# Optimization experiments

Measured on AMD Instinct MI355X. Metric: run time of the kernel, lower is better.

Reference implementation:

```python
import jax, jax.numpy as jnp
import numpy as np

SCALING = 128.0 / 64  # alpha / rank = 2.0
EPS = 1e-8


def setup_inputs() -> dict:
    key = jax.random.key(0)
    ks = jax.random.split(key, 5)
    B, S, D_IN, D_OUT, R = 2, 4096, 4096, 4096, 64
    x = jax.random.normal(ks[0], (B, S, D_IN), dtype=jnp.float32)
    base_output = jax.random.normal(ks[1], (B, S, D_OUT), dtype=jnp.float32)
    base_weight = jax.random.normal(ks[2], (D_OUT, D_IN), dtype=jnp.float32) * 0.02
    lora_A = jax.random.normal(ks[3], (R, D_IN), dtype=jnp.float32) * 0.02
    lora_B = jax.random.normal(ks[4], (D_OUT, R), dtype=jnp.float32) * 0.02
    magnitude = jnp.ones((D_OUT,), dtype=jnp.float32)
    return {"x": x, "base_output": base_output, "base_weight": base_weight,
            "lora_A": lora_A, "lora_B": lora_B, "magnitude": magnitude}


def reference(x, base_output, base_weight, lora_A, lora_B, magnitude):
    # LoRA path: x @ A^T @ B^T, scaled  (dropout p=0 -> identity)
    xa = jnp.einsum('bsd,rd->bsr', x, lora_A)          # [B,S,r]
    delta_v = jnp.einsum('bsr,or->bso', xa, lora_B) * SCALING  # [B,S,out]
    # Updated weight and its per-row L2 norm
    updated_weight = base_weight + (lora_B @ lora_A) * SCALING  # [out,in]
    updated_norm = jnp.sqrt(jnp.sum(updated_weight * updated_weight, axis=1))  # [out]
    mag_scale = magnitude / (updated_norm + EPS)  # [out]
    combined = base_output + delta_v
    return combined * mag_scale[None, None, :]
```

## Files before the change

### kernel.cpp

```cpp
#include <hip/hip_runtime.h>
#include <math.h>

typedef __bf16 bf16x8 __attribute__((ext_vector_type(8)));
typedef float f32x4 __attribute__((ext_vector_type(4)));

#define MFMA16(a, b, c) __builtin_amdgcn_mfma_f32_16x16x32_bf16(a, b, c, 0, 0, 0)

static constexpr int M_TOT = 8192;
static constexpr int DIN = 4096;
static constexpr int DOUT = 4096;
static constexpr int RNK = 64;

__device__ inline unsigned short f2bf(float f) {
    union { float f; unsigned u; } v; v.f = f;
    unsigned r = v.u + 0x7FFFu + ((v.u >> 16) & 1u);
    return (unsigned short)(r >> 16);
}

__global__ __launch_bounds__(256) void k_prep(const float* __restrict__ A,
                                              const float* __restrict__ B,
                                              unsigned short* __restrict__ Afrag,
                                              unsigned short* __restrict__ Atfrag,
                                              unsigned short* __restrict__ Bfrag) {
    int i = blockIdx.x * 256 + threadIdx.x;
    unsigned short ab = f2bf(A[i]);
    int n = i >> 12, k = i & 4095;
    Afrag[(((k >> 5) << 2) + (n >> 4)) * 512 +
          ((((k >> 3) & 3) << 4) + (n & 15)) * 8 + (k & 7)] = ab;
    Atfrag[(((k >> 4) << 1) + (n >> 5)) * 512 +
           ((((n >> 3) & 3) << 4) + (k & 15)) * 8 + (n & 7)] = ab;
    unsigned short bb = f2bf(B[i]);
    int o = i >> 6, r = i & 63;
    Bfrag[(((o >> 4) << 1) + (r >> 5)) * 512 +
          ((((r >> 3) & 3) << 4) + (o & 15)) * 8 + (r & 7)] = bb;
}

__global__ __launch_bounds__(256, 4) void k1_xa(const float* __restrict__ x,
                                                const unsigned short* __restrict__ Afrag,
                                                float* __restrict__ pxa) {
    __shared__ __align__(16) char smem[33024];
    unsigned short (*stage)[1032] = (unsigned short (*)[1032])smem;
    float (*red)[1024] = (float (*)[1024])smem;
    int tid = threadIdx.x;
    int wid = tid >> 6, lane = tid & 63;
    int row = lane & 15, kq = lane >> 4;
    int lane8 = lane * 8;
    int mt = blockIdx.x & 511, kpart = blockIdx.x >> 9;
    int m0 = mt * 16;
    int sr = tid >> 4, sc = (tid & 15) * 4;

    const float* xp = x + (size_t)(m0 + sr) * DIN + kpart * 1024 + sc;
    f32x4 r[16];
    #pragma unroll
    for (int p = 0; p < 16; ++p) r[p] = *(const f32x4*)(xp + p * 64);

    #pragma unroll
    for (int p = 0; p < 16; ++p) {
        ushort4 h;
        h.x = f2bf(r[p][0]); h.y = f2bf(r[p][1]); h.z = f2bf(r[p][2]); h.w = f2bf(r[p][3]);
        *(ushort4*)&stage[sr][p * 64 + sc] = h;
    }
    __syncthreads();

    f32x4 acc0 = {0.f, 0.f, 0.f, 0.f};
    f32x4 acc1 = acc0, acc2 = acc0, acc3 = acc0;
    #pragma unroll
    for (int s = 0; s < 8; ++s) {
        bf16x8 af = *(const bf16x8*)&stage[row][wid * 256 + s * 32 + kq * 8];
        int ks = kpart * 32 + wid * 8 + s;
        const unsigned short* ap = Afrag + (size_t)(ks << 2) * 512 + lane8;
        acc0 = MFMA16(af, *(const bf16x8*)(ap), acc0);
        acc1 = MFMA16(af, *(const bf16x8*)(ap + 512), acc1);
        acc2 = MFMA16(af, *(const bf16x8*)(ap + 1024), acc2);
        acc3 = MFMA16(af, *(const bf16x8*)(ap + 1536), acc3);
    }
    __syncthreads();

    int mb = kq * 4;
    #pragma unroll
    for (int rg = 0; rg < 4; ++rg) {
        red[wid][(mb + rg) * 64 + row]      = acc0[rg];
        red[wid][(mb + rg) * 64 + 16 + row] = acc1[rg];
        red[wid][(mb + rg) * 64 + 32 + row] = acc2[rg];
        red[wid][(mb + rg) * 64 + 48 + row] = acc3[rg];
    }
    __syncthreads();
    #pragma unroll
    for (int e = tid; e < 1024; e += 256) {
        float s = red[0][e] + red[1][e] + red[2][e] + red[3][e];
        pxa[(size_t)kpart * M_TOT * RNK + (size_t)(m0 + (e >> 6)) * RNK + (e & 63)] = s;
    }
}

__global__ __launch_bounds__(256) void k1_fin(const float* __restrict__ pxa,
                                              unsigned short* __restrict__ xafrag) {
    int tid = threadIdx.x;
    int mt = blockIdx.x;
    int e0 = tid * 4;
    size_t o = (size_t)(mt * 16 + (e0 >> 6)) * RNK + (e0 & 63);
    f32x4 s0 = *(const f32x4*)(pxa + o);
    f32x4 s1 = *(const f32x4*)(pxa + (size_t)M_TOT * RNK + o);
    f32x4 s2 = *(const f32x4*)(pxa + 2 * (size_t)M_TOT * RNK + o);
    f32x4 s3 = *(const f32x4*)(pxa + 3 * (size_t)M_TOT * RNK + o);
    int ml = e0 >> 6, r0 = e0 & 63;
    ushort4 h;
    h.x = f2bf(s0[0] + s1[0] + s2[0] + s3[0]);
    h.y = f2bf(s0[1] + s1[1] + s2[1] + s3[1]);
    h.z = f2bf(s0[2] + s1[2] + s2[2] + s3[2]);
    h.w = f2bf(s0[3] + s1[3] + s2[3] + s3[3]);
    *(ushort4*)&xafrag[((size_t)(mt * 2 + (r0 >> 5))) * 512 +
                       ((((r0 >> 3) & 3) << 4) + ml) * 8 + (r0 & 7)] = h;
}

__global__ __launch_bounds__(256, 4) void k2_norm(const float* __restrict__ bw,
                                                  const unsigned short* __restrict__ Bfrag,
                                                  const unsigned short* __restrict__ Atfrag,
                                                  float* __restrict__ pn) {
    __shared__ __align__(16) char smem[33280];
    float (*stagef)[516] = (float (*)[516])smem;
    float (*part)[16] = (float (*)[16])(smem + 33024);
    int tid = threadIdx.x;
    int wid = tid >> 6, lane = tid & 63;
    int row = lane & 15, kq = lane >> 4;
    int lane8 = lane * 8;
    int ot = blockIdx.x & 255, ipart = blockIdx.x >> 8;
    int o0 = ot * 16;
    int sr = tid >> 4, sc = (tid & 15) * 4;

    const float* bwp = bw + (size_t)(o0 + sr) * DIN + ipart * 512 + sc;
    f32x4 q[8];
    #pragma unroll
    for (int p = 0; p < 8; ++p) q[p] = *(const f32x4*)(bwp + p * 64);

    bf16x8 b0 = *(const bf16x8*)(Bfrag + (size_t)(ot * 2) * 512 + lane8);
    bf16x8 b1 = *(const bf16x8*)(Bfrag + (size_t)(ot * 2 + 1) * 512 + lane8);

    #pragma unroll
    for (int p = 0; p < 8; ++p) *(f32x4*)&stagef[sr][p * 64 + sc] = q[p];
    __syncthreads();

    f32x4 nacc = {0.f, 0.f, 0.f, 0.f};
    #pragma unroll
    for (int g = 0; g < 8; ++g) {
        int iloc = wid * 128 + g * 16;
        int it = (ipart * 512 + iloc) >> 4;
        const unsigned short* atp = Atfrag + (size_t)(it * 2) * 512 + lane8;
        bf16x8 a0 = *(const bf16x8*)(atp);
        bf16x8 a1 = *(const bf16x8*)(atp + 512);
        f32x4 d = {0.f, 0.f, 0.f, 0.f};
        d = MFMA16(a0, b0, d);
        d = MFMA16(a1, b1, d);
        f32x4 wv = *(const f32x4*)&stagef[row][iloc + kq * 4];
        #pragma unroll
        for (int rg = 0; rg < 4; ++rg) {
            float w = wv[rg] + 2.0f * d[rg];
            nacc[rg] += w * w;
        }
    }
    float ns = nacc[0] + nacc[1] + nacc[2] + nacc[3];
    ns += __shfl_xor(ns, 16, 64);
    ns += __shfl_xor(ns, 32, 64);
    if (kq == 0) part[wid][row] = ns;
    __syncthreads();
    if (tid < 16)
        pn[ipart * DOUT + o0 + tid] =
            part[0][tid] + part[1][tid] + part[2][tid] + part[3][tid];
}

__global__ __launch_bounds__(256) void k2b_scale(const float* __restrict__ pn,
                                                 const float* __restrict__ mag,
                                                 float* __restrict__ mscale) {
    int o = blockIdx.x * 256 + threadIdx.x;
    float n2 = 0.f;
    #pragma unroll
    for (int p = 0; p < 8; ++p) n2 += pn[p * DOUT + o];
    mscale[o] = mag[o] / (sqrtf(n2) + 1e-8f);
}

__global__ __launch_bounds__(256) void kB(const float* __restrict__ base,
                                          const unsigned short* __restrict__ xafrag,
                                          const unsigned short* __restrict__ Bfrag,
                                          const float* __restrict__ mscale,
                                          float* __restrict__ out) {
    __shared__ float dls[32][260];
    int tid = threadIdx.x;
    int wid = tid >> 6, lane = tid & 63;
    int row = lane & 15, kq = lane >> 4;
    int m0 = blockIdx.x * 32;
    int n0 = blockIdx.y * 256;
    int col = n0 + lane * 4;
    int lane8 = lane * 8;

    f32x4 bpre[2][4];
    #pragma unroll
    for (int h = 0; h < 2; ++h)
        #pragma unroll
        for (int r = 0; r < 4; ++r)
            bpre[h][r] = __builtin_nontemporal_load(
                (const f32x4*)(base + (size_t)(m0 + h * 16 + wid * 4 + r) * DOUT + col));
    f32x4 msv = *(const f32x4*)(mscale + col);

    bf16x8 xb0[2], xb1[2];
    #pragma unroll
    for (int h = 0; h < 2; ++h) {
        size_t mt = (size_t)(blockIdx.x * 2 + h);
        xb0[h] = *(const bf16x8*)(xafrag + (mt * 2) * 512 + lane8);
        xb1[h] = *(const bf16x8*)(xafrag + (mt * 2 + 1) * 512 + lane8);
    }

    #pragma unroll
    for (int nt = 0; nt < 4; ++nt) {
        size_t ntg = (size_t)((n0 + wid * 64 + nt * 16) >> 4);
        bf16x8 a0 = *(const bf16x8*)(Bfrag + (ntg * 2) * 512 + lane8);
        bf16x8 a1 = *(const bf16x8*)(Bfrag + (ntg * 2 + 1) * 512 + lane8);
        #pragma unroll
        for (int h = 0; h < 2; ++h) {
            f32x4 acc = {0.f, 0.f, 0.f, 0.f};
            acc = MFMA16(a0, xb0[h], acc);
            acc = MFMA16(a1, xb1[h], acc);
            *(f32x4*)&dls[h * 16 + row][wid * 64 + nt * 16 + kq * 4] = acc;
        }
    }
    __syncthreads();

    #pragma unroll
    for (int h = 0; h < 2; ++h)
        #pragma unroll
        for (int r = 0; r < 4; ++r) {
            int m = h * 16 + wid * 4 + r;
            f32x4 d = *(const f32x4*)&dls[m][lane * 4];
            size_t gidx = (size_t)(m0 + m) * DOUT + col;
            f32x4 o;
            #pragma unroll
            for (int j = 0; j < 4; ++j) o[j] = (bpre[h][r][j] + 2.0f * d[j]) * msv[j];
            __builtin_nontemporal_store(o, (f32x4*)(out + gidx));
        }
}

extern "C" void kernel_launch(void* const* d_in, const int* in_sizes, int n_in,
                              void* d_out, int out_size, void* d_ws, size_t ws_size,
                              hipStream_t stream) {
    const float* x    = (const float*)d_in[0];
    const float* base = (const float*)d_in[1];
    const float* bw   = (const float*)d_in[2];
    const float* lA   = (const float*)d_in[3];
    const float* lB   = (const float*)d_in[4];
    const float* mag  = (const float*)d_in[5];
    float* out = (float*)d_out;

    char* ws = (char*)d_ws;
    unsigned short* Afrag  = (unsigned short*)(ws);
    unsigned short* Atfrag = (unsigned short*)(ws + (512u << 10));
    unsigned short* Bfrag  = (unsigned short*)(ws + (1024u << 10));
    unsigned short* xafrag = (unsigned short*)(ws + (1536u << 10));
    float*          pxa    = (float*)(ws + (2560u << 10));
    float*          pn     = (float*)(ws + (10752u << 10));
    float*          msc    = (float*)(ws + (10880u << 10));

    hipLaunchKernelGGL(k_prep, dim3(1024), dim3(256), 0, stream, lA, lB, Afrag, Atfrag, Bfrag);
    hipLaunchKernelGGL(k1_xa, dim3(2048), dim3(256), 0, stream, x, Afrag, pxa);
    hipLaunchKernelGGL(k2_norm, dim3(2048), dim3(256), 0, stream, bw, Bfrag, Atfrag, pn);
    hipLaunchKernelGGL(k1_fin, dim3(512), dim3(256), 0, stream, pxa, xafrag);
    hipLaunchKernelGGL(k2b_scale, dim3(DOUT / 256), dim3(256), 0, stream, pn, mag, msc);
    hipLaunchKernelGGL(kB, dim3(M_TOT / 32, DOUT / 256), dim3(256), 0, stream,
                       base, xafrag, Bfrag, msc, out);
}
```

Measured before the change: 124.0 us.

## Halve split-K in xa and norm kernels with register-prefetched chunk loop

k1_xa and k2_norm now cover twice the K range per block in four chunks, loading the next chunk into registers while the current chunk's MFMAs run. The split-K factor drops from 4 to 2 for xa and from 8 to 4 for the norm, so fewer partial sums are written and re-read by the finalize kernels. Shared memory per block is halved. The cost is half as many blocks (1024 each), an extra barrier per chunk, and the occupancy hint removed from launch_bounds.

```diff
diff --git a/kernel.cpp b/kernel.cpp
--- a/kernel.cpp
+++ b/kernel.cpp
@@ -35,11 +35,11 @@
           ((((r >> 3) & 3) << 4) + (o & 15)) * 8 + (r & 7)] = bb;
 }
 
-__global__ __launch_bounds__(256, 4) void k1_xa(const float* __restrict__ x,
-                                                const unsigned short* __restrict__ Afrag,
-                                                float* __restrict__ pxa) {
-    __shared__ __align__(16) char smem[33024];
-    unsigned short (*stage)[1032] = (unsigned short (*)[1032])smem;
+__global__ __launch_bounds__(256) void k1_xa(const float* __restrict__ x,
+                                             const unsigned short* __restrict__ Afrag,
+                                             float* __restrict__ pxa) {
+    __shared__ __align__(16) char smem[16640];
+    unsigned short (*stage)[520] = (unsigned short (*)[520])smem;
     float (*red)[1024] = (float (*)[1024])smem;
     int tid = threadIdx.x;
     int wid = tid >> 6, lane = tid & 63;
@@ -49,30 +49,40 @@
     int m0 = mt * 16;
     int sr = tid >> 4, sc = (tid & 15) * 4;
 
-    const float* xp = x + (size_t)(m0 + sr) * DIN + kpart * 1024 + sc;
-    f32x4 r[16];
-    #pragma unroll
-    for (int p = 0; p < 16; ++p) r[p] = *(const f32x4*)(xp + p * 64);
-
-    #pragma unroll
-    for (int p = 0; p < 16; ++p) {
-        ushort4 h;
-        h.x = f2bf(r[p][0]); h.y = f2bf(r[p][1]); h.z = f2bf(r[p][2]); h.w = f2bf(r[p][3]);
-        *(ushort4*)&stage[sr][p * 64 + sc] = h;
-    }
-    __syncthreads();
+    const float* xp = x + (size_t)(m0 + sr) * DIN + kpart * 2048 + sc;
+
+    f32x4 r[8];
+    #pragma unroll
+    for (int p = 0; p < 8; ++p) r[p] = *(const f32x4*)(xp + p * 64);
 
     f32x4 acc0 = {0.f, 0.f, 0.f, 0.f};
     f32x4 acc1 = acc0, acc2 = acc0, acc3 = acc0;
-    #pragma unroll
-    for (int s = 0; s < 8; ++s) {
-        bf16x8 af = *(const bf16x8*)&stage[row][wid * 256 + s * 32 + kq * 8];
-        int ks = kpart * 32 + wid * 8 + s;
-        const unsigned short* ap = Afrag + (size_t)(ks << 2) * 512 + lane8;
-        acc0 = MFMA16(af, *(const bf16x8*)(ap), acc0);
-        acc1 = MFMA16(af, *(const bf16x8*)(ap + 512), acc1);
-        acc2 = MFMA16(af, *(const bf16x8*)(ap + 1024), acc2);
-        acc3 = MFMA16(af, *(const bf16x8*)(ap + 1536), acc3);
+
+    for (int c = 0; c < 4; ++c) {
+        __syncthreads();
+        #pragma unroll
+        for (int p = 0; p < 8; ++p) {
+            ushort4 h;
+            h.x = f2bf(r[p][0]); h.y = f2bf(r[p][1]);
+            h.z = f2bf(r[p][2]); h.w = f2bf(r[p][3]);
+            *(ushort4*)&stage[sr][p * 64 + sc] = h;
+        }
+        __syncthreads();
+        if (c < 3) {
+            const float* nx = xp + (c + 1) * 512;
+            #pragma unroll
+            for (int p = 0; p < 8; ++p) r[p] = *(const f32x4*)(nx + p * 64);
+        }
+        #pragma unroll
+        for (int s = 0; s < 4; ++s) {
+            bf16x8 af = *(const bf16x8*)&stage[row][wid * 128 + s * 32 + kq * 8];
+            int ks = (kpart * 2048 + c * 512 + wid * 128 + s * 32) >> 5;
+            const unsigned short* ap = Afrag + (size_t)(ks << 2) * 512 + lane8;
+            acc0 = MFMA16(af, *(const bf16x8*)(ap), acc0);
+            acc1 = MFMA16(af, *(const bf16x8*)(ap + 512), acc1);
+            acc2 = MFMA16(af, *(const bf16x8*)(ap + 1024), acc2);
+            acc3 = MFMA16(af, *(const bf16x8*)(ap + 1536), acc3);
+        }
     }
     __syncthreads();
 
@@ -100,25 +110,23 @@
     size_t o = (size_t)(mt * 16 + (e0 >> 6)) * RNK + (e0 & 63);
     f32x4 s0 = *(const f32x4*)(pxa + o);
     f32x4 s1 = *(const f32x4*)(pxa + (size_t)M_TOT * RNK + o);
-    f32x4 s2 = *(const f32x4*)(pxa + 2 * (size_t)M_TOT * RNK + o);
-    f32x4 s3 = *(const f32x4*)(pxa + 3 * (size_t)M_TOT * RNK + o);
     int ml = e0 >> 6, r0 = e0 & 63;
     ushort4 h;
-    h.x = f2bf(s0[0] + s1[0] + s2[0] + s3[0]);
-    h.y = f2bf(s0[1] + s1[1] + s2[1] + s3[1]);
-    h.z = f2bf(s0[2] + s1[2] + s2[2] + s3[2]);
-    h.w = f2bf(s0[3] + s1[3] + s2[3] + s3[3]);
+    h.x = f2bf(s0[0] + s1[0]);
+    h.y = f2bf(s0[1] + s1[1]);
+    h.z = f2bf(s0[2] + s1[2]);
+    h.w = f2bf(s0[3] + s1[3]);
     *(ushort4*)&xafrag[((size_t)(mt * 2 + (r0 >> 5))) * 512 +
                        ((((r0 >> 3) & 3) << 4) + ml) * 8 + (r0 & 7)] = h;
 }
 
-__global__ __launch_bounds__(256, 4) void k2_norm(const float* __restrict__ bw,
-                                                  const unsigned short* __restrict__ Bfrag,
-                                                  const unsigned short* __restrict__ Atfrag,
-                                                  float* __restrict__ pn) {
-    __shared__ __align__(16) char smem[33280];
-    float (*stagef)[516] = (float (*)[516])smem;
-    float (*part)[16] = (float (*)[16])(smem + 33024);
+__global__ __launch_bounds__(256) void k2_norm(const float* __restrict__ bw,
+                                               const unsigned short* __restrict__ Bfrag,
+                                               const unsigned short* __restrict__ Atfrag,
+                                               float* __restrict__ pn) {
+    __shared__ __align__(16) char smem[16896];
+    float (*stagef)[260] = (float (*)[260])smem;
+    float (*part)[16] = (float (*)[16])(smem + 16640);
     int tid = threadIdx.x;
     int wid = tid >> 6, lane = tid & 63;
     int row = lane & 15, kq = lane >> 4;
@@ -127,34 +135,43 @@
     int o0 = ot * 16;
     int sr = tid >> 4, sc = (tid & 15) * 4;
 
-    const float* bwp = bw + (size_t)(o0 + sr) * DIN + ipart * 512 + sc;
-    f32x4 q[8];
-    #pragma unroll
-    for (int p = 0; p < 8; ++p) q[p] = *(const f32x4*)(bwp + p * 64);
+    const float* bwp = bw + (size_t)(o0 + sr) * DIN + ipart * 1024 + sc;
+
+    f32x4 q[4];
+    #pragma unroll
+    for (int p = 0; p < 4; ++p) q[p] = *(const f32x4*)(bwp + p * 64);
 
     bf16x8 b0 = *(const bf16x8*)(Bfrag + (size_t)(ot * 2) * 512 + lane8);
     bf16x8 b1 = *(const bf16x8*)(Bfrag + (size_t)(ot * 2 + 1) * 512 + lane8);
 
-    #pragma unroll
-    for (int p = 0; p < 8; ++p) *(f32x4*)&stagef[sr][p * 64 + sc] = q[p];
-    __syncthreads();
-
     f32x4 nacc = {0.f, 0.f, 0.f, 0.f};
-    #pragma unroll
-    for (int g = 0; g < 8; ++g) {
-        int iloc = wid * 128 + g * 16;
-        int it = (ipart * 512 + iloc) >> 4;
-        const unsigned short* atp = Atfrag + (size_t)(it * 2) * 512 + lane8;
-        bf16x8 a0 = *(const bf16x8*)(atp);
-        bf16x8 a1 = *(const bf16x8*)(atp + 512);
-        f32x4 d = {0.f, 0.f, 0.f, 0.f};
-        d = MFMA16(a0, b0, d);
-        d = MFMA16(a1, b1, d);
-        f32x4 wv = *(const f32x4*)&stagef[row][iloc + kq * 4];
-        #pragma unroll
-        for (int rg = 0; rg < 4; ++rg) {
-            float w = wv[rg] + 2.0f * d[rg];
-            nacc[rg] += w * w;
+
+    for (int c = 0; c < 4; ++c) {
+        __syncthreads();
+        #pragma unroll
+        for (int p = 0; p < 4; ++p) *(f32x4*)&stagef[sr][p * 64 + sc] = q[p];
+        __syncthreads();
+        if (c < 3) {
+            const float* nb = bwp + (c + 1) * 256;
+            #pragma unroll
+            for (int p = 0; p < 4; ++p) q[p] = *(const f32x4*)(nb + p * 64);
+        }
+        #pragma unroll
+        for (int g = 0; g < 4; ++g) {
+            int iloc = wid * 64 + g * 16;
+            int it = (ipart * 1024 + c * 256 + iloc) >> 4;
+            const unsigned short* atp = Atfrag + (size_t)(it * 2) * 512 + lane8;
+            bf16x8 a0 = *(const bf16x8*)(atp);
+            bf16x8 a1 = *(const bf16x8*)(atp + 512);
+            f32x4 d = {0.f, 0.f, 0.f, 0.f};
+            d = MFMA16(a0, b0, d);
+            d = MFMA16(a1, b1, d);
+            f32x4 wv = *(const f32x4*)&stagef[row][iloc + kq * 4];
+            #pragma unroll
+            for (int rg = 0; rg < 4; ++rg) {
+                float w = wv[rg] + 2.0f * d[rg];
+                nacc[rg] += w * w;
+            }
         }
     }
     float ns = nacc[0] + nacc[1] + nacc[2] + nacc[3];
@@ -173,7 +190,7 @@
     int o = blockIdx.x * 256 + threadIdx.x;
     float n2 = 0.f;
     #pragma unroll
-    for (int p = 0; p < 8; ++p) n2 += pn[p * DOUT + o];
+    for (int p = 0; p < 4; ++p) n2 += pn[p * DOUT + o];
     mscale[o] = mag[o] / (sqrtf(n2) + 1e-8f);
 }
 
@@ -254,12 +271,12 @@
     unsigned short* Bfrag  = (unsigned short*)(ws + (1024u << 10));
     unsigned short* xafrag = (unsigned short*)(ws + (1536u << 10));
     float*          pxa    = (float*)(ws + (2560u << 10));
-    float*          pn     = (float*)(ws + (10752u << 10));
-    float*          msc    = (float*)(ws + (10880u << 10));
+    float*          pn     = (float*)(ws + (6656u << 10));
+    float*          msc    = (float*)(ws + (6720u << 10));
 
     hipLaunchKernelGGL(k_prep, dim3(1024), dim3(256), 0, stream, lA, lB, Afrag, Atfrag, Bfrag);
-    hipLaunchKernelGGL(k1_xa, dim3(2048), dim3(256), 0, stream, x, Afrag, pxa);
-    hipLaunchKernelGGL(k2_norm, dim3(2048), dim3(256), 0, stream, bw, Bfrag, Atfrag, pn);
+    hipLaunchKernelGGL(k1_xa, dim3(1024), dim3(256), 0, stream, x, Afrag, pxa);
+    hipLaunchKernelGGL(k2_norm, dim3(1024), dim3(256), 0, stream, bw, Bfrag, Atfrag, pn);
     hipLaunchKernelGGL(k1_fin, dim3(512), dim3(256), 0, stream, pxa, xafrag);
     hipLaunchKernelGGL(k2b_scale, dim3(DOUT / 256), dim3(256), 0, stream, pn, mag, msc);
     hipLaunchKernelGGL(kB, dim3(M_TOT / 32, DOUT / 256), dim3(256), 0, stream,
```

After: 119.3 us. -3.8%, faster.

## Merge xA and norm kernels into one interleaved launch, drop LDS staging

Applied to the files above, without the earlier changes.

The x@A^T partial kernel and the weight-norm partial kernel are fused into one launch, with even blocks doing xA and odd blocks doing norm work. The two small finalize kernels are merged into a second launch. The LDS staging of x and base_weight is removed: each lane now loads its MFMA operand directly from global memory and converts to bf16 in registers. This cuts launch count and lets the two memory-bound phases overlap, at the risk of less coalesced global reads and a lost occupancy hint.

```diff
diff --git a/kernel.cpp b/kernel.cpp
--- a/kernel.cpp
+++ b/kernel.cpp
@@ -35,146 +35,124 @@
           ((((r >> 3) & 3) << 4) + (o & 15)) * 8 + (r & 7)] = bb;
 }
 
-__global__ __launch_bounds__(256, 4) void k1_xa(const float* __restrict__ x,
-                                                const unsigned short* __restrict__ Afrag,
-                                                float* __restrict__ pxa) {
-    __shared__ __align__(16) char smem[33024];
-    unsigned short (*stage)[1032] = (unsigned short (*)[1032])smem;
-    float (*red)[1024] = (float (*)[1024])smem;
+__global__ __launch_bounds__(256) void kAB(const float* __restrict__ x,
+                                           const unsigned short* __restrict__ Afrag,
+                                           float* __restrict__ pxa,
+                                           const float* __restrict__ bw,
+                                           const unsigned short* __restrict__ Bfrag,
+                                           const unsigned short* __restrict__ Atfrag,
+                                           float* __restrict__ pn) {
+    __shared__ __align__(16) float red[4][1024];
     int tid = threadIdx.x;
     int wid = tid >> 6, lane = tid & 63;
     int row = lane & 15, kq = lane >> 4;
     int lane8 = lane * 8;
-    int mt = blockIdx.x & 511, kpart = blockIdx.x >> 9;
-    int m0 = mt * 16;
-    int sr = tid >> 4, sc = (tid & 15) * 4;
-
-    const float* xp = x + (size_t)(m0 + sr) * DIN + kpart * 1024 + sc;
-    f32x4 r[16];
-    #pragma unroll
-    for (int p = 0; p < 16; ++p) r[p] = *(const f32x4*)(xp + p * 64);
-
-    #pragma unroll
-    for (int p = 0; p < 16; ++p) {
+    int sub = blockIdx.x >> 1;
+
+    if ((blockIdx.x & 1) == 0) {
+        int mt = sub & 511, kpart = sub >> 9;
+        int m0 = mt * 16;
+        const float* xrow = x + (size_t)(m0 + row) * DIN;
+
+        f32x4 acc0 = {0.f, 0.f, 0.f, 0.f};
+        f32x4 acc1 = acc0, acc2 = acc0, acc3 = acc0;
+
+        #pragma unroll
+        for (int s = 0; s < 8; ++s) {
+            int k = kpart * 1024 + wid * 256 + s * 32 + kq * 8;
+            f32x4 xlo = *(const f32x4*)(xrow + k);
+            f32x4 xhi = *(const f32x4*)(xrow + k + 4);
+            int ks = (kpart * 1024 + wid * 256 + s * 32) >> 5;
+            const unsigned short* ap = Afrag + (size_t)ks * 2048 + lane8;
+            bf16x8 af;
+            #pragma unroll
+            for (int j = 0; j < 4; ++j) { af[j] = (__bf16)xlo[j]; af[j + 4] = (__bf16)xhi[j]; }
+            acc0 = MFMA16(af, *(const bf16x8*)(ap), acc0);
+            acc1 = MFMA16(af, *(const bf16x8*)(ap + 512), acc1);
+            acc2 = MFMA16(af, *(const bf16x8*)(ap + 1024), acc2);
+            acc3 = MFMA16(af, *(const bf16x8*)(ap + 1536), acc3);
+        }
+
+        int mb = kq * 4;
+        #pragma unroll
+        for (int rg = 0; rg < 4; ++rg) {
+            red[wid][(mb + rg) * 64 + row]      = acc0[rg];
+            red[wid][(mb + rg) * 64 + 16 + row] = acc1[rg];
+            red[wid][(mb + rg) * 64 + 32 + row] = acc2[rg];
+            red[wid][(mb + rg) * 64 + 48 + row] = acc3[rg];
+        }
+        __syncthreads();
+        #pragma unroll
+        for (int e = tid; e < 1024; e += 256) {
+            float s = red[0][e] + red[1][e] + red[2][e] + red[3][e];
+            pxa[(size_t)kpart * M_TOT * RNK + (size_t)(m0 + (e >> 6)) * RNK + (e & 63)] = s;
+        }
+    } else {
+        int ot = sub & 255, ipart = sub >> 8;
+        int o0 = ot * 16;
+        const float* bwrow = bw + (size_t)(o0 + row) * DIN;
+
+        bf16x8 b0 = *(const bf16x8*)(Bfrag + (size_t)(ot * 2) * 512 + lane8);
+        bf16x8 b1 = *(const bf16x8*)(Bfrag + (size_t)(ot * 2 + 1) * 512 + lane8);
+
+        f32x4 nacc = {0.f, 0.f, 0.f, 0.f};
+        #pragma unroll
+        for (int g = 0; g < 8; ++g) {
+            int i0 = ipart * 512 + wid * 128 + g * 16;
+            int it = i0 >> 4;
+            const unsigned short* atp = Atfrag + (size_t)it * 1024 + lane8;
+            bf16x8 a0 = *(const bf16x8*)(atp);
+            bf16x8 a1 = *(const bf16x8*)(atp + 512);
+            f32x4 d = {0.f, 0.f, 0.f, 0.f};
+            d = MFMA16(a0, b0, d);
+            d = MFMA16(a1, b1, d);
+            f32x4 wv = *(const f32x4*)(bwrow + i0 + kq * 4);
+            #pragma unroll
+            for (int rg = 0; rg < 4; ++rg) {
+                float w = wv[rg] + 2.0f * d[rg];
+                nacc[rg] += w * w;
+            }
+        }
+        float ns = nacc[0] + nacc[1] + nacc[2] + nacc[3];
+        ns += __shfl_xor(ns, 16, 64);
+        ns += __shfl_xor(ns, 32, 64);
+        if (kq == 0) red[0][wid * 16 + row] = ns;
+        __syncthreads();
+        if (tid < 16)
+            pn[ipart * DOUT + o0 + tid] = red[0][tid] + red[0][16 + tid] +
+                                          red[0][32 + tid] + red[0][48 + tid];
+    }
+}
+
+__global__ __launch_bounds__(256) void kfin(const float* __restrict__ pxa,
+                                            unsigned short* __restrict__ xafrag,
+                                            const float* __restrict__ pn,
+                                            const float* __restrict__ mag,
+                                            float* __restrict__ mscale) {
+    int tid = threadIdx.x;
+    if (blockIdx.x < 512) {
+        int mt = blockIdx.x;
+        int e0 = tid * 4;
+        size_t o = (size_t)(mt * 16 + (e0 >> 6)) * RNK + (e0 & 63);
+        f32x4 s0 = *(const f32x4*)(pxa + o);
+        f32x4 s1 = *(const f32x4*)(pxa + (size_t)M_TOT * RNK + o);
+        f32x4 s2 = *(const f32x4*)(pxa + 2 * (size_t)M_TOT * RNK + o);
+        f32x4 s3 = *(const f32x4*)(pxa + 3 * (size_t)M_TOT * RNK + o);
+        int ml = e0 >> 6, r0 = e0 & 63;
         ushort4 h;
-        h.x = f2bf(r[p][0]); h.y = f2bf(r[p][1]); h.z = f2bf(r[p][2]); h.w = f2bf(r[p][3]);
-        *(ushort4*)&stage[sr][p * 64 + sc] = h;
-    }
-    __syncthreads();
-
-    f32x4 acc0 = {0.f, 0.f, 0.f, 0.f};
-    f32x4 acc1 = acc0, acc2 = acc0, acc3 = acc0;
-    #pragma unroll
-    for (int s = 0; s < 8; ++s) {
-        bf16x8 af = *(const bf16x8*)&stage[row][wid * 256 + s * 32 + kq * 8];
-        int ks = kpart * 32 + wid * 8 + s;
-        const unsigned short* ap = Afrag + (size_t)(ks << 2) * 512 + lane8;
-        acc0 = MFMA16(af, *(const bf16x8*)(ap), acc0);
-        acc1 = MFMA16(af, *(const bf16x8*)(ap + 512), acc1);
-        acc2 = MFMA16(af, *(const bf16x8*)(ap + 1024), acc2);
-        acc3 = MFMA16(af, *(const bf16x8*)(ap + 1536), acc3);
-    }
-    __syncthreads();
-
-    int mb = kq * 4;
-    #pragma unroll
-    for (int rg = 0; rg < 4; ++rg) {
-        red[wid][(mb + rg) * 64 + row]      = acc0[rg];
-        red[wid][(mb + rg) * 64 + 16 + row] = acc1[rg];
-        red[wid][(mb + rg) * 64 + 32 + row] = acc2[rg];
-        red[wid][(mb + rg) * 64 + 48 + row] = acc3[rg];
-    }
-    __syncthreads();
-    #pragma unroll
-    for (int e = tid; e < 1024; e += 256) {
-        float s = red[0][e] + red[1][e] + red[2][e] + red[3][e];
-        pxa[(size_t)kpart * M_TOT * RNK + (size_t)(m0 + (e >> 6)) * RNK + (e & 63)] = s;
-    }
-}
-
-__global__ __launch_bounds__(256) void k1_fin(const float* __restrict__ pxa,
-                                              unsigned short* __restrict__ xafrag) {
-    int tid = threadIdx.x;
-    int mt = blockIdx.x;
-    int e0 = tid * 4;
-    size_t o = (size_t)(mt * 16 + (e0 >> 6)) * RNK + (e0 & 63);
-    f32x4 s0 = *(const f32x4*)(pxa + o);
-    f32x4 s1 = *(const f32x4*)(pxa + (size_t)M_TOT * RNK + o);
-    f32x4 s2 = *(const f32x4*)(pxa + 2 * (size_t)M_TOT * RNK + o);
-    f32x4 s3 = *(const f32x4*)(pxa + 3 * (size_t)M_TOT * RNK + o);
-    int ml = e0 >> 6, r0 = e0 & 63;
-    ushort4 h;
-    h.x = f2bf(s0[0] + s1[0] + s2[0] + s3[0]);
-    h.y = f2bf(s0[1] + s1[1] + s2[1] + s3[1]);
-    h.z = f2bf(s0[2] + s1[2] + s2[2] + s3[2]);
-    h.w = f2bf(s0[3] + s1[3] + s2[3] + s3[3]);
-    *(ushort4*)&xafrag[((size_t)(mt * 2 + (r0 >> 5))) * 512 +
-                       ((((r0 >> 3) & 3) << 4) + ml) * 8 + (r0 & 7)] = h;
-}
-
-__global__ __launch_bounds__(256, 4) void k2_norm(const float* __restrict__ bw,
-                                                  const unsigned short* __restrict__ Bfrag,
-                                                  const unsigned short* __restrict__ Atfrag,
-                                                  float* __restrict__ pn) {
-    __shared__ __align__(16) char smem[33280];
-    float (*stagef)[516] = (float (*)[516])smem;
-    float (*part)[16] = (float (*)[16])(smem + 33024);
-    int tid = threadIdx.x;
-    int wid = tid >> 6, lane = tid & 63;
-    int row = lane & 15, kq = lane >> 4;
-    int lane8 = lane * 8;
-    int ot = blockIdx.x & 255, ipart = blockIdx.x >> 8;
-    int o0 = ot * 16;
-    int sr = tid >> 4, sc = (tid & 15) * 4;
-
-    const float* bwp = bw + (size_t)(o0 + sr) * DIN + ipart * 512 + sc;
-    f32x4 q[8];
-    #pragma unroll
-    for (int p = 0; p < 8; ++p) q[p] = *(const f32x4*)(bwp + p * 64);
-
-    bf16x8 b0 = *(const bf16x8*)(Bfrag + (size_t)(ot * 2) * 512 + lane8);
-    bf16x8 b1 = *(const bf16x8*)(Bfrag + (size_t)(ot * 2 + 1) * 512 + lane8);
-
-    #pragma unroll
-    for (int p = 0; p < 8; ++p) *(f32x4*)&stagef[sr][p * 64 + sc] = q[p];
-    __syncthreads();
-
-    f32x4 nacc = {0.f, 0.f, 0.f, 0.f};
-    #pragma unroll
-    for (int g = 0; g < 8; ++g) {
-        int iloc = wid * 128 + g * 16;
-        int it = (ipart * 512 + iloc) >> 4;
-        const unsigned short* atp = Atfrag + (size_t)(it * 2) * 512 + lane8;
-        bf16x8 a0 = *(const bf16x8*)(atp);
-        bf16x8 a1 = *(const bf16x8*)(atp + 512);
-        f32x4 d = {0.f, 0.f, 0.f, 0.f};
-        d = MFMA16(a0, b0, d);
-        d = MFMA16(a1, b1, d);
-        f32x4 wv = *(const f32x4*)&stagef[row][iloc + kq * 4];
-        #pragma unroll
-        for (int rg = 0; rg < 4; ++rg) {
-            float w = wv[rg] + 2.0f * d[rg];
-            nacc[rg] += w * w;
-        }
-    }
-    float ns = nacc[0] + nacc[1] + nacc[2] + nacc[3];
-    ns += __shfl_xor(ns, 16, 64);
-    ns += __shfl_xor(ns, 32, 64);
-    if (kq == 0) part[wid][row] = ns;
-    __syncthreads();
-    if (tid < 16)
-        pn[ipart * DOUT + o0 + tid] =
-            part[0][tid] + part[1][tid] + part[2][tid] + part[3][tid];
-}
-
-__global__ __launch_bounds__(256) void k2b_scale(const float* __restrict__ pn,
-                                                 const float* __restrict__ mag,
-                                                 float* __restrict__ mscale) {
-    int o = blockIdx.x * 256 + threadIdx.x;
-    float n2 = 0.f;
-    #pragma unroll
-    for (int p = 0; p < 8; ++p) n2 += pn[p * DOUT + o];
-    mscale[o] = mag[o] / (sqrtf(n2) + 1e-8f);
+        h.x = f2bf(s0[0] + s1[0] + s2[0] + s3[0]);
+        h.y = f2bf(s0[1] + s1[1] + s2[1] + s3[1]);
+        h.z = f2bf(s0[2] + s1[2] + s2[2] + s3[2]);
+        h.w = f2bf(s0[3] + s1[3] + s2[3] + s3[3]);
+        *(ushort4*)&xafrag[((size_t)(mt * 2 + (r0 >> 5))) * 512 +
+                           ((((r0 >> 3) & 3) << 4) + ml) * 8 + (r0 & 7)] = h;
+    } else {
+        int o = (int)(blockIdx.x - 512) * 256 + tid;
+        float n2 = 0.f;
+        #pragma unroll
+        for (int p = 0; p < 8; ++p) n2 += pn[p * DOUT + o];
+        mscale[o] = mag[o] / (sqrtf(n2) + 1e-8f);
+    }
 }
 
 __global__ __launch_bounds__(256) void kB(const float* __restrict__ base,
@@ -258,10 +236,9 @@
     float*          msc    = (float*)(ws + (10880u << 10));
 
     hipLaunchKernelGGL(k_prep, dim3(1024), dim3(256), 0, stream, lA, lB, Afrag, Atfrag, Bfrag);
-    hipLaunchKernelGGL(k1_xa, dim3(2048), dim3(256), 0, stream, x, Afrag, pxa);
-    hipLaunchKernelGGL(k2_norm, dim3(2048), dim3(256), 0, stream, bw, Bfrag, Atfrag, pn);
-    hipLaunchKernelGGL(k1_fin, dim3(512), dim3(256), 0, stream, pxa, xafrag);
-    hipLaunchKernelGGL(k2b_scale, dim3(DOUT / 256), dim3(256), 0, stream, pn, mag, msc);
+    hipLaunchKernelGGL(kAB, dim3(4096), dim3(256), 0, stream,
+                       x, Afrag, pxa, bw, Bfrag, Atfrag, pn);
+    hipLaunchKernelGGL(kfin, dim3(528), dim3(256), 0, stream, pxa, xafrag, pn, mag, msc);
     hipLaunchKernelGGL(kB, dim3(M_TOT / 32, DOUT / 256), dim3(256), 0, stream,
                        base, xafrag, Bfrag, msc, out);
 }
```

Result: faster. 120.4 us (-2.9%).
